# Kernel optimization log

Measured on AMD Instinct MI355X. Metric: run time of the kernel, lower is better.

Reference implementation:

```python
import jax, jax.numpy as jnp
import numpy as np

B, T, D = 4, 4096, 1024
P = 64  # d_model / n_head

def setup_inputs() -> dict:
    key = jax.random.key(0)
    k1, k2, k3 = jax.random.split(key, 3)
    x = jax.random.normal(k1, (B, T, D), dtype=jnp.float32)
    Wqkv = jax.random.normal(k2, (D, 3 * P), dtype=jnp.float32) * (1.0 / np.sqrt(D))
    bqkv = jax.random.normal(k3, (3 * P,), dtype=jnp.float32) * 0.01
    return {"x": x, "Wqkv": Wqkv, "bqkv": bqkv}

def reference(x, Wqkv, bqkv):
    Bv, Tv, Cv = x.shape
    qkv = (x @ Wqkv + bqkv).reshape(Bv, Tv, 3, P)  # [B,T,3,p]
    q, k, v = qkv[:, :, 0, :], qkv[:, :, 1, :], qkv[:, :, 2, :]
    # raw scores (source applies NO 1/sqrt(p) scaling)
    S = jnp.einsum('btp,bsp->bts', q, k)  # [B,T,T]
    causal = jnp.tril(jnp.ones((Tv, Tv), dtype=bool))
    S = jnp.where(causal[None, :, :], S, jnp.float32(-jnp.inf))
    Pm = jax.nn.softmax(S, axis=-1)
    O = jnp.einsum('bts,bsp->btp', Pm, v)  # [B,T,p]
    return O
```

## Files before the change

kernel.cpp:

```cpp
#include <hip/hip_runtime.h>
#include <hip/hip_fp16.h>

#define B_ 4
#define T_ 4096
#define D_ 1024

typedef _Float16 h8 __attribute__((ext_vector_type(8)));
typedef _Float16 h4 __attribute__((ext_vector_type(4)));
typedef float f32x4 __attribute__((ext_vector_type(4)));

#define LOG2E 1.44269504088896340736f
#define MASKV -3.0e38f
#define MINIT -1.0e30f
#define EXP2(x) __builtin_amdgcn_exp2f(x)

__global__ __launch_bounds__(256) void wt_kernel(const float* __restrict__ W,
                                                 _Float16* __restrict__ Wt) {
    __shared__ _Float16 Tr[192][20];
    const int tid = threadIdx.x, k0 = blockIdx.x * 16;
#pragma unroll
    for (int i = 0; i < 3; i++) {
        int fi = tid + 256 * i;
        int r = fi / 48, c4 = fi % 48;
        float4 v = *(const float4*)(W + (size_t)(k0 + r) * 192 + c4 * 4);
        Tr[c4 * 4 + 0][r] = (_Float16)v.x;
        Tr[c4 * 4 + 1][r] = (_Float16)v.y;
        Tr[c4 * 4 + 2][r] = (_Float16)v.z;
        Tr[c4 * 4 + 3][r] = (_Float16)v.w;
    }
    __syncthreads();
#pragma unroll
    for (int i = 0; i < 3; i++) {
        int oi = tid + 256 * i;
        int n = oi >> 2, kq = oi & 3;
        *(h4*)(Wt + (size_t)n * D_ + k0 + kq * 4) = *(const h4*)&Tr[n][kq * 4];
    }
}

__global__ __launch_bounds__(256) void proj_kernel(
    const float* __restrict__ x, const _Float16* __restrict__ Wt,
    const float* __restrict__ bias,
    _Float16* __restrict__ qh, _Float16* __restrict__ kh, _Float16* __restrict__ vh)
{
    __shared__ _Float16 As[2][32][40];
    __shared__ _Float16 Bs[2][192][40];
    __shared__ _Float16 Ost[32][200];
    const int tid = threadIdx.x;
    const int w = tid >> 6, lane = tid & 63, quad = lane >> 4, l16 = lane & 15;
    const int row0 = blockIdx.x * 32;
    const int mstrip = w & 1;
    const int ngrp = (w >> 1) * 6;

    float bvals[6];
#pragma unroll
    for (int nt = 0; nt < 6; nt++) bvals[nt] = bias[(ngrp + nt) * 16 + l16];

    f32x4 acc[6];
#pragma unroll
    for (int i = 0; i < 6; i++) acc[i] = (f32x4){0.f, 0.f, 0.f, 0.f};

    const int arow = tid >> 3, ac0 = (tid & 7) * 4;

    float4 xa;
    h8 wreg[3];
    {
        xa = *(const float4*)(x + (size_t)(row0 + arow) * D_ + ac0);
#pragma unroll
        for (int p = 0; p < 3; p++) {
            int f = tid + 256 * p; int n = f >> 2, c0 = (f & 3) * 8;
            wreg[p] = *(const h8*)(Wt + (size_t)n * D_ + c0);
        }
    }

    for (int kc = 0; kc < 32; kc++) {
        const int buf = kc & 1;
        h4 av;
        av[0]=(_Float16)xa.x; av[1]=(_Float16)xa.y; av[2]=(_Float16)xa.z; av[3]=(_Float16)xa.w;
        *(h4*)&As[buf][arow][ac0] = av;
#pragma unroll
        for (int p = 0; p < 3; p++) {
            int f = tid + 256 * p; int n = f >> 2, c0 = (f & 3) * 8;
            *(h8*)&Bs[buf][n][c0] = wreg[p];
        }
        if (kc + 1 < 32) {
            int k0 = (kc + 1) * 32;
            xa = *(const float4*)(x + (size_t)(row0 + arow) * D_ + k0 + ac0);
#pragma unroll
            for (int p = 0; p < 3; p++) {
                int f = tid + 256 * p; int n = f >> 2, c0 = (f & 3) * 8;
                wreg[p] = *(const h8*)(Wt + (size_t)n * D_ + k0 + c0);
            }
        }
        __syncthreads();
        h8 a0 = *(const h8*)&As[buf][16 * mstrip + l16][quad * 8];
#pragma unroll
        for (int nt = 0; nt < 6; nt++) {
            h8 b0 = *(const h8*)&Bs[buf][(ngrp + nt) * 16 + l16][quad * 8];
            acc[nt] = __builtin_amdgcn_mfma_f32_16x16x32_f16(a0, b0, acc[nt], 0, 0, 0);
        }
    }

#pragma unroll
    for (int nt = 0; nt < 6; nt++) {
        int n = (ngrp + nt) * 16 + l16;
        float scale = (n < 64) ? LOG2E : 1.0f;
#pragma unroll
        for (int reg = 0; reg < 4; reg++)
            Ost[16 * mstrip + quad * 4 + reg][n] =
                (_Float16)((acc[nt][reg] + bvals[nt]) * scale);
    }
    __syncthreads();
    {
        const int mrow = tid >> 3, c0 = (tid & 7) * 8;
        _Float16* dsts[3] = {qh, kh, vh};
#pragma unroll
        for (int g = 0; g < 3; g++)
            *(h8*)(dsts[g] + (size_t)(row0 + mrow) * 64 + c0) =
                *(const h8*)&Ost[mrow][g * 64 + c0];
    }
}

__global__ __launch_bounds__(256, 4) void attn_kernel(
    const _Float16* __restrict__ qh, const _Float16* __restrict__ kh,
    const _Float16* __restrict__ vh, float* __restrict__ out,
    _Float16* __restrict__ Opart, float2* __restrict__ ml,
    int lgC, int NC1, int direct, int q8, int total)
{
    __shared__ _Float16 Ks[2][64][72];
    __shared__ _Float16 Vt[2][64][72];
    const int tid = threadIdx.x;
    const int w = tid >> 6, lane = tid & 63, quad = lane >> 4, l16 = lane & 15;
    const int C = 1 << lgC;

    const int bid = blockIdx.x;
    const int cid = (bid & 7) * q8 + (bid >> 3);
    if (cid >= total) return;

    const int b = cid / NC1;
    int rem = cid - b * NC1;
    int qt2 = 0, k0 = 0, cnt = 1;
    for (int i = 0; i < 32; i++) {
        int nc = (2 * i + 2 + C - 1) >> lgC;
        if (rem < nc) { qt2 = i; k0 = rem << lgC; cnt = min(C, 2 * i + 2 - k0); break; }
        rem -= nc;
    }
    const size_t base = (size_t)b * T_ * 64;
    const int qbase = qt2 * 128 + w * 32;

    h8 qf[2][2];
#pragma unroll
    for (int u = 0; u < 2; u++) {
        const _Float16* qp = qh + base + (size_t)(qbase + u * 16 + l16) * 64 + quad * 8;
        qf[u][0] = *(const h8*)qp;
        qf[u][1] = *(const h8*)(qp + 32);
    }

    f32x4 o[8];
#pragma unroll
    for (int i = 0; i < 8; i++) o[i] = (f32x4){0.f, 0.f, 0.f, 0.f};
    float m[2] = {MINIT, MINIT}, l[2] = {0.f, 0.f};

    const int krow = tid >> 3, kc0 = (tid & 7) * 8;
    const int vp0 = (tid & 15) * 4, vc0 = (tid >> 4) * 4;
    h8 kreg[2];
    h4 vreg[4];
    {
        const _Float16* kp = kh + base + (size_t)(k0 * 64) * 64;
        kreg[0] = *(const h8*)(kp + (size_t)krow * 64 + kc0);
        kreg[1] = *(const h8*)(kp + (size_t)(krow + 32) * 64 + kc0);
        const _Float16* vp = vh + base + (size_t)(k0 * 64 + vc0) * 64 + vp0;
#pragma unroll
        for (int i = 0; i < 4; i++) vreg[i] = *(const h4*)(vp + (size_t)i * 64);
    }

    const int kend = k0 + cnt;
    for (int kt = k0; kt < kend; kt++) {
        const int buf = kt & 1;
        *(h8*)&Ks[buf][krow][kc0] = kreg[0];
        *(h8*)&Ks[buf][krow + 32][kc0] = kreg[1];
#pragma unroll
        for (int j = 0; j < 4; j++) {
            h4 t;
            t[0] = vreg[0][j]; t[1] = vreg[1][j]; t[2] = vreg[2][j]; t[3] = vreg[3][j];
            *(h4*)&Vt[buf][vp0 + j][vc0] = t;
        }
        if (kt + 1 < kend) {
            const _Float16* kp = kh + base + (size_t)((kt + 1) * 64) * 64;
            kreg[0] = *(const h8*)(kp + (size_t)krow * 64 + kc0);
            kreg[1] = *(const h8*)(kp + (size_t)(krow + 32) * 64 + kc0);
            const _Float16* vp = vh + base + (size_t)((kt + 1) * 64 + vc0) * 64 + vp0;
#pragma unroll
            for (int i = 0; i < 4; i++) vreg[i] = *(const h4*)(vp + (size_t)i * 64);
        }
        __syncthreads();

        const bool skip = (kt * 64) > (qbase + 31);
        if (!skip) {
            f32x4 s[2][4];
#pragma unroll
            for (int nt = 0; nt < 4; nt++) {
                h8 kf0 = *(const h8*)&Ks[buf][nt * 16 + l16][quad * 8];
                h8 kf1 = *(const h8*)&Ks[buf][nt * 16 + l16][32 + quad * 8];
#pragma unroll
                for (int u = 0; u < 2; u++) {
                    f32x4 c = (f32x4){0.f, 0.f, 0.f, 0.f};
                    c = __builtin_amdgcn_mfma_f32_16x16x32_f16(kf0, qf[u][0], c, 0, 0, 0);
                    c = __builtin_amdgcn_mfma_f32_16x16x32_f16(kf1, qf[u][1], c, 0, 0, 0);
                    s[u][nt] = c;
                }
            }

            h4 pf[2][4];
#pragma unroll
            for (int u = 0; u < 2; u++) {
                const int qrow = qbase + u * 16 + l16;
                if (kt * 64 + 63 > qbase + u * 16) {
#pragma unroll
                    for (int nt = 0; nt < 4; nt++)
#pragma unroll
                        for (int reg = 0; reg < 4; reg++) {
                            int sg = kt * 64 + nt * 16 + quad * 4 + reg;
                            if (sg > qrow) s[u][nt][reg] = MASKV;
                        }
                }
                float mx = s[u][0][0];
#pragma unroll
                for (int nt = 0; nt < 4; nt++)
#pragma unroll
                    for (int reg = 0; reg < 4; reg++) mx = fmaxf(mx, s[u][nt][reg]);
                mx = fmaxf(mx, __shfl_xor(mx, 16));
                mx = fmaxf(mx, __shfl_xor(mx, 32));
                float mnew = fmaxf(m[u], mx);
                float alpha = EXP2(m[u] - mnew);
                m[u] = mnew;
                float rs = 0.f;
#pragma unroll
                for (int nt = 0; nt < 4; nt++) {
#pragma unroll
                    for (int reg = 0; reg < 4; reg++) {
                        float p = EXP2(s[u][nt][reg] - mnew);
                        s[u][nt][reg] = p;
                        rs += p;
                    }
                    h4 ph;
                    ph[0]=(_Float16)s[u][nt][0]; ph[1]=(_Float16)s[u][nt][1];
                    ph[2]=(_Float16)s[u][nt][2]; ph[3]=(_Float16)s[u][nt][3];
                    pf[u][nt] = ph;
                }
                rs += __shfl_xor(rs, 16);
                rs += __shfl_xor(rs, 32);
                l[u] = l[u] * alpha + rs;
#pragma unroll
                for (int pt = 0; pt < 4; pt++)
#pragma unroll
                    for (int reg = 0; reg < 4; reg++) o[u * 4 + pt][reg] *= alpha;
            }

#pragma unroll
            for (int pt = 0; pt < 4; pt++)
#pragma unroll
                for (int nt = 0; nt < 4; nt++) {
                    h4 vf = *(const h4*)&Vt[buf][pt * 16 + l16][nt * 16 + quad * 4];
                    o[pt]     = __builtin_amdgcn_mfma_f32_16x16x16f16(vf, pf[0][nt], o[pt], 0, 0, 0);
                    o[4 + pt] = __builtin_amdgcn_mfma_f32_16x16x16f16(vf, pf[1][nt], o[4 + pt], 0, 0, 0);
                }
        }
    }

    if (direct) {
#pragma unroll
        for (int u = 0; u < 2; u++) {
            float linv = 1.0f / l[u];
            int trow = qt2 * 128 + w * 32 + u * 16 + l16;
#pragma unroll
            for (int pt = 0; pt < 4; pt++)
#pragma unroll
                for (int reg = 0; reg < 4; reg++)
                    out[base + (size_t)trow * 64 + pt * 16 + quad * 4 + reg] =
                        o[u * 4 + pt][reg] * linv;
        }
    } else {
        __syncthreads();
        _Float16* St = &Ks[0][0][0];
#pragma unroll
        for (int u = 0; u < 2; u++) {
            int r = w * 32 + u * 16 + l16;
#pragma unroll
            for (int pt = 0; pt < 4; pt++) {
                h4 ph;
#pragma unroll
                for (int reg = 0; reg < 4; reg++) ph[reg] = (_Float16)o[u * 4 + pt][reg];
                *(h4*)&St[r * 72 + pt * 16 + quad * 4] = ph;
            }
            if (quad == 0) ml[(size_t)cid * 128 + r] = make_float2(m[u], l[u]);
        }
        __syncthreads();
        _Float16* op = Opart + (size_t)cid * 8192;
        const int r = tid >> 1, c0 = (tid & 1) * 32;
#pragma unroll
        for (int j = 0; j < 4; j++)
            *(h8*)(op + r * 64 + c0 + 8 * j) = *(const h8*)&St[r * 72 + c0 + 8 * j];
    }
}

__global__ __launch_bounds__(256) void combine_kernel(
    const _Float16* __restrict__ Opart, const float2* __restrict__ ml,
    float* __restrict__ out, int lgC, int NC1)
{
    const int C = 1 << lgC;
    const int task = blockIdx.x;
    const int b = task >> 8, tile = (task >> 3) & 31, rg = task & 7;
    int pref = 0;
    for (int i = 0; i < tile; i++) pref += (2 * i + 2 + C - 1) >> lgC;
    const int cbase = b * NC1 + pref;
    const int nch = (2 * tile + 2 + C - 1) >> lgC;

    const int r = rg * 16 + (threadIdx.x >> 4);
    const int c0 = (threadIdx.x & 15) * 4;

    float M = MINIT;
    for (int i = 0; i < nch; i++) M = fmaxf(M, ml[(size_t)(cbase + i) * 128 + r].x);
    float L = 0.f, acc[4] = {0.f, 0.f, 0.f, 0.f};
    for (int i = 0; i < nch; i++) {
        float2 v = ml[(size_t)(cbase + i) * 128 + r];
        float sc = EXP2(v.x - M);
        L += sc * v.y;
        h4 x4 = *(const h4*)(Opart + (size_t)(cbase + i) * 8192 + (size_t)r * 64 + c0);
#pragma unroll
        for (int t = 0; t < 4; t++) acc[t] += sc * (float)x4[t];
    }
    float inv = 1.0f / L;
    float4 res = { acc[0]*inv, acc[1]*inv, acc[2]*inv, acc[3]*inv };
    *(float4*)(out + ((size_t)b * T_ + tile * 128 + r) * 64 + c0) = res;
}

extern "C" void kernel_launch(void* const* d_in, const int* in_sizes, int n_in,
                              void* d_out, int out_size, void* d_ws, size_t ws_size,
                              hipStream_t stream) {
    const float* x    = (const float*)d_in[0];
    const float* W    = (const float*)d_in[1];
    const float* bias = (const float*)d_in[2];
    float* out = (float*)d_out;
    char* ws = (char*)d_ws;
    _Float16* qh = (_Float16*)(ws);
    _Float16* kh = (_Float16*)(ws + (size_t)2 * 1024 * 1024);
    _Float16* vh = (_Float16*)(ws + (size_t)4 * 1024 * 1024);
    _Float16* Wt = (_Float16*)(ws + (size_t)6 * 1024 * 1024);
    const size_t pbase = (size_t)8 * 1024 * 1024;

    int lgC = -1, nc1 = 32;
    for (int lg = 3; lg <= 6; lg++) {
        int C = 1 << lg, n1 = 0;
        for (int i = 0; i < 32; i++) n1 += (2 * i + 2 + C - 1) >> lg;
        size_t need = pbase + (size_t)4 * n1 * (8192 * 2 + 128 * 8);
        if (need <= ws_size) { lgC = lg; nc1 = n1; break; }
    }
    int direct = (lgC < 0) ? 1 : 0;
    if (direct) { lgC = 6; nc1 = 32; }
    _Float16* Opart = (_Float16*)(ws + pbase);
    float2*   mlp   = (float2*)(ws + pbase + (size_t)4 * nc1 * 8192 * 2);

    const int total = 4 * nc1;
    const int q8 = (total + 7) / 8;

    wt_kernel<<<64, 256, 0, stream>>>(W, Wt);
    proj_kernel<<<512, 256, 0, stream>>>(x, Wt, bias, qh, kh, vh);
    attn_kernel<<<8 * q8, 256, 0, stream>>>(qh, kh, vh, out, Opart, mlp,
                                            lgC, nc1, direct, q8, total);
    if (!direct)
        combine_kernel<<<1024, 256, 0, stream>>>(Opart, mlp, out, lgC, nc1);
}
```

Before: 166.6 us.

## Shrink attention query tile to 64 rows and load K fragments directly into registers

The attention kernel now gives each block 64 query rows (16 per wave) instead of 128, removes the shared-memory K buffer, and has each lane load its K MFMA fragments straight from global memory with a one-tile register prefetch. Split-KV chunking, the partial-output layout and the combine kernel are reindexed for 64-row tiles, and the chunk-size search now starts at 4 tiles. This is meant to cut LDS traffic and the K staging stores, balance the causal work more finely and allow more blocks. In exchange, each K tile is read from global or L2 by every wave instead of once per block, and each block covers fewer query rows, so K/V reuse drops.

```diff
diff --git a/kernel.cpp b/kernel.cpp
--- a/kernel.cpp
+++ b/kernel.cpp
@@ -126,7 +126,6 @@
     _Float16* __restrict__ Opart, float2* __restrict__ ml,
     int lgC, int NC1, int direct, int q8, int total)
 {
-    __shared__ _Float16 Ks[2][64][72];
     __shared__ _Float16 Vt[2][64][72];
     const int tid = threadIdx.x;
     const int w = tid >> 6, lane = tid & 63, quad = lane >> 4, l16 = lane & 15;
@@ -138,46 +137,49 @@
 
     const int b = cid / NC1;
     int rem = cid - b * NC1;
-    int qt2 = 0, k0 = 0, cnt = 1;
-    for (int i = 0; i < 32; i++) {
-        int nc = (2 * i + 2 + C - 1) >> lgC;
-        if (rem < nc) { qt2 = i; k0 = rem << lgC; cnt = min(C, 2 * i + 2 - k0); break; }
+    int qt = 0, k0 = 0, cnt = 1;
+    for (int q = 0; q < 64; q++) {
+        int nc = (q + C) >> lgC;
+        if (rem < nc) { qt = q; k0 = rem << lgC; cnt = min(C, q + 1 - k0); break; }
         rem -= nc;
     }
     const size_t base = (size_t)b * T_ * 64;
-    const int qbase = qt2 * 128 + w * 32;
-
-    h8 qf[2][2];
-#pragma unroll
-    for (int u = 0; u < 2; u++) {
-        const _Float16* qp = qh + base + (size_t)(qbase + u * 16 + l16) * 64 + quad * 8;
-        qf[u][0] = *(const h8*)qp;
-        qf[u][1] = *(const h8*)(qp + 32);
-    }
-
-    f32x4 o[8];
-#pragma unroll
-    for (int i = 0; i < 8; i++) o[i] = (f32x4){0.f, 0.f, 0.f, 0.f};
-    float m[2] = {MINIT, MINIT}, l[2] = {0.f, 0.f};
-
-    const int krow = tid >> 3, kc0 = (tid & 7) * 8;
+    const int qbase = qt * 64 + w * 16;
+
+    h8 qf[2];
+    {
+        const _Float16* qp = qh + base + (size_t)(qbase + l16) * 64 + quad * 8;
+        qf[0] = *(const h8*)qp;
+        qf[1] = *(const h8*)(qp + 32);
+    }
+
+    f32x4 o[4];
+#pragma unroll
+    for (int i = 0; i < 4; i++) o[i] = (f32x4){0.f, 0.f, 0.f, 0.f};
+    float m = MINIT, l = 0.f;
+
     const int vp0 = (tid & 15) * 4, vc0 = (tid >> 4) * 4;
-    h8 kreg[2];
     h4 vreg[4];
     {
-        const _Float16* kp = kh + base + (size_t)(k0 * 64) * 64;
-        kreg[0] = *(const h8*)(kp + (size_t)krow * 64 + kc0);
-        kreg[1] = *(const h8*)(kp + (size_t)(krow + 32) * 64 + kc0);
         const _Float16* vp = vh + base + (size_t)(k0 * 64 + vc0) * 64 + vp0;
 #pragma unroll
         for (int i = 0; i < 4; i++) vreg[i] = *(const h4*)(vp + (size_t)i * 64);
+    }
+
+    const _Float16* kbase = kh + base + (size_t)l16 * 64 + quad * 8;
+    h8 kf[4][2];
+    {
+        const _Float16* kp = kbase + (size_t)k0 * 64 * 64;
+#pragma unroll
+        for (int nt = 0; nt < 4; nt++) {
+            kf[nt][0] = *(const h8*)(kp + (size_t)nt * 16 * 64);
+            kf[nt][1] = *(const h8*)(kp + (size_t)nt * 16 * 64 + 32);
+        }
     }
 
     const int kend = k0 + cnt;
     for (int kt = k0; kt < kend; kt++) {
         const int buf = kt & 1;
-        *(h8*)&Ks[buf][krow][kc0] = kreg[0];
-        *(h8*)&Ks[buf][krow + 32][kc0] = kreg[1];
 #pragma unroll
         for (int j = 0; j < 4; j++) {
             h4 t;
@@ -185,121 +187,108 @@
             *(h4*)&Vt[buf][vp0 + j][vc0] = t;
         }
         if (kt + 1 < kend) {
-            const _Float16* kp = kh + base + (size_t)((kt + 1) * 64) * 64;
-            kreg[0] = *(const h8*)(kp + (size_t)krow * 64 + kc0);
-            kreg[1] = *(const h8*)(kp + (size_t)(krow + 32) * 64 + kc0);
             const _Float16* vp = vh + base + (size_t)((kt + 1) * 64 + vc0) * 64 + vp0;
 #pragma unroll
             for (int i = 0; i < 4; i++) vreg[i] = *(const h4*)(vp + (size_t)i * 64);
         }
         __syncthreads();
 
-        const bool skip = (kt * 64) > (qbase + 31);
-        if (!skip) {
-            f32x4 s[2][4];
+        f32x4 s[4];
+#pragma unroll
+        for (int nt = 0; nt < 4; nt++) {
+            f32x4 c = (f32x4){0.f, 0.f, 0.f, 0.f};
+            c = __builtin_amdgcn_mfma_f32_16x16x32_f16(kf[nt][0], qf[0], c, 0, 0, 0);
+            c = __builtin_amdgcn_mfma_f32_16x16x32_f16(kf[nt][1], qf[1], c, 0, 0, 0);
+            s[nt] = c;
+        }
+        if (kt + 1 < kend) {
+            const _Float16* kp = kbase + (size_t)(kt + 1) * 64 * 64;
 #pragma unroll
             for (int nt = 0; nt < 4; nt++) {
-                h8 kf0 = *(const h8*)&Ks[buf][nt * 16 + l16][quad * 8];
-                h8 kf1 = *(const h8*)&Ks[buf][nt * 16 + l16][32 + quad * 8];
-#pragma unroll
-                for (int u = 0; u < 2; u++) {
-                    f32x4 c = (f32x4){0.f, 0.f, 0.f, 0.f};
-                    c = __builtin_amdgcn_mfma_f32_16x16x32_f16(kf0, qf[u][0], c, 0, 0, 0);
-                    c = __builtin_amdgcn_mfma_f32_16x16x32_f16(kf1, qf[u][1], c, 0, 0, 0);
-                    s[u][nt] = c;
+                kf[nt][0] = *(const h8*)(kp + (size_t)nt * 16 * 64);
+                kf[nt][1] = *(const h8*)(kp + (size_t)nt * 16 * 64 + 32);
+            }
+        }
+
+        if (kt == qt) {
+            const int qrow = w * 16 + l16;
+#pragma unroll
+            for (int nt = 0; nt < 4; nt++)
+#pragma unroll
+                for (int reg = 0; reg < 4; reg++) {
+                    int sg = nt * 16 + quad * 4 + reg;
+                    if (sg > qrow) s[nt][reg] = MASKV;
                 }
-            }
-
-            h4 pf[2][4];
-#pragma unroll
-            for (int u = 0; u < 2; u++) {
-                const int qrow = qbase + u * 16 + l16;
-                if (kt * 64 + 63 > qbase + u * 16) {
-#pragma unroll
-                    for (int nt = 0; nt < 4; nt++)
-#pragma unroll
-                        for (int reg = 0; reg < 4; reg++) {
-                            int sg = kt * 64 + nt * 16 + quad * 4 + reg;
-                            if (sg > qrow) s[u][nt][reg] = MASKV;
-                        }
-                }
-                float mx = s[u][0][0];
-#pragma unroll
-                for (int nt = 0; nt < 4; nt++)
-#pragma unroll
-                    for (int reg = 0; reg < 4; reg++) mx = fmaxf(mx, s[u][nt][reg]);
-                mx = fmaxf(mx, __shfl_xor(mx, 16));
-                mx = fmaxf(mx, __shfl_xor(mx, 32));
-                float mnew = fmaxf(m[u], mx);
-                float alpha = EXP2(m[u] - mnew);
-                m[u] = mnew;
-                float rs = 0.f;
-#pragma unroll
-                for (int nt = 0; nt < 4; nt++) {
-#pragma unroll
-                    for (int reg = 0; reg < 4; reg++) {
-                        float p = EXP2(s[u][nt][reg] - mnew);
-                        s[u][nt][reg] = p;
-                        rs += p;
-                    }
-                    h4 ph;
-                    ph[0]=(_Float16)s[u][nt][0]; ph[1]=(_Float16)s[u][nt][1];
-                    ph[2]=(_Float16)s[u][nt][2]; ph[3]=(_Float16)s[u][nt][3];
-                    pf[u][nt] = ph;
-                }
-                rs += __shfl_xor(rs, 16);
-                rs += __shfl_xor(rs, 32);
-                l[u] = l[u] * alpha + rs;
-#pragma unroll
-                for (int pt = 0; pt < 4; pt++)
-#pragma unroll
-                    for (int reg = 0; reg < 4; reg++) o[u * 4 + pt][reg] *= alpha;
-            }
-
-#pragma unroll
-            for (int pt = 0; pt < 4; pt++)
-#pragma unroll
-                for (int nt = 0; nt < 4; nt++) {
-                    h4 vf = *(const h4*)&Vt[buf][pt * 16 + l16][nt * 16 + quad * 4];
-                    o[pt]     = __builtin_amdgcn_mfma_f32_16x16x16f16(vf, pf[0][nt], o[pt], 0, 0, 0);
-                    o[4 + pt] = __builtin_amdgcn_mfma_f32_16x16x16f16(vf, pf[1][nt], o[4 + pt], 0, 0, 0);
-                }
-        }
+        }
+
+        float mx = s[0][0];
+#pragma unroll
+        for (int nt = 0; nt < 4; nt++)
+#pragma unroll
+            for (int reg = 0; reg < 4; reg++) mx = fmaxf(mx, s[nt][reg]);
+        mx = fmaxf(mx, __shfl_xor(mx, 16));
+        mx = fmaxf(mx, __shfl_xor(mx, 32));
+        float mnew = fmaxf(m, mx);
+        float alpha = EXP2(m - mnew);
+        m = mnew;
+        float rs = 0.f;
+        h4 pf[4];
+#pragma unroll
+        for (int nt = 0; nt < 4; nt++) {
+            h4 ph;
+#pragma unroll
+            for (int reg = 0; reg < 4; reg++) {
+                float p = EXP2(s[nt][reg] - mnew);
+                rs += p;
+                ph[reg] = (_Float16)p;
+            }
+            pf[nt] = ph;
+        }
+        rs += __shfl_xor(rs, 16);
+        rs += __shfl_xor(rs, 32);
+        l = l * alpha + rs;
+#pragma unroll
+        for (int pt = 0; pt < 4; pt++)
+#pragma unroll
+            for (int reg = 0; reg < 4; reg++) o[pt][reg] *= alpha;
+
+#pragma unroll
+        for (int pt = 0; pt < 4; pt++)
+#pragma unroll
+            for (int nt = 0; nt < 4; nt++) {
+                h4 vf = *(const h4*)&Vt[buf][pt * 16 + l16][nt * 16 + quad * 4];
+                o[pt] = __builtin_amdgcn_mfma_f32_16x16x16f16(vf, pf[nt], o[pt], 0, 0, 0);
+            }
     }
 
     if (direct) {
-#pragma unroll
-        for (int u = 0; u < 2; u++) {
-            float linv = 1.0f / l[u];
-            int trow = qt2 * 128 + w * 32 + u * 16 + l16;
-#pragma unroll
-            for (int pt = 0; pt < 4; pt++)
-#pragma unroll
-                for (int reg = 0; reg < 4; reg++)
-                    out[base + (size_t)trow * 64 + pt * 16 + quad * 4 + reg] =
-                        o[u * 4 + pt][reg] * linv;
-        }
+        float linv = 1.0f / l;
+        int trow = qt * 64 + w * 16 + l16;
+#pragma unroll
+        for (int pt = 0; pt < 4; pt++)
+#pragma unroll
+            for (int reg = 0; reg < 4; reg++)
+                out[base + (size_t)trow * 64 + pt * 16 + quad * 4 + reg] =
+                    o[pt][reg] * linv;
     } else {
         __syncthreads();
-        _Float16* St = &Ks[0][0][0];
-#pragma unroll
-        for (int u = 0; u < 2; u++) {
-            int r = w * 32 + u * 16 + l16;
+        _Float16* St = &Vt[0][0][0];
+        {
+            int r = w * 16 + l16;
 #pragma unroll
             for (int pt = 0; pt < 4; pt++) {
                 h4 ph;
 #pragma unroll
-                for (int reg = 0; reg < 4; reg++) ph[reg] = (_Float16)o[u * 4 + pt][reg];
+                for (int reg = 0; reg < 4; reg++) ph[reg] = (_Float16)o[pt][reg];
                 *(h4*)&St[r * 72 + pt * 16 + quad * 4] = ph;
             }
-            if (quad == 0) ml[(size_t)cid * 128 + r] = make_float2(m[u], l[u]);
+            if (quad == 0) ml[(size_t)cid * 64 + r] = make_float2(m, l);
         }
         __syncthreads();
-        _Float16* op = Opart + (size_t)cid * 8192;
-        const int r = tid >> 1, c0 = (tid & 1) * 32;
-#pragma unroll
-        for (int j = 0; j < 4; j++)
-            *(h8*)(op + r * 64 + c0 + 8 * j) = *(const h8*)&St[r * 72 + c0 + 8 * j];
+        _Float16* op = Opart + (size_t)cid * 4096;
+        const int r = tid >> 2, c0 = (tid & 3) * 16;
+        *(h8*)(op + r * 64 + c0)     = *(const h8*)&St[r * 72 + c0];
+        *(h8*)(op + r * 64 + c0 + 8) = *(const h8*)&St[r * 72 + c0 + 8];
     }
 }
 
@@ -309,29 +298,29 @@
 {
     const int C = 1 << lgC;
     const int task = blockIdx.x;
-    const int b = task >> 8, tile = (task >> 3) & 31, rg = task & 7;
+    const int b = task >> 8, qt = (task >> 2) & 63, rg = task & 3;
     int pref = 0;
-    for (int i = 0; i < tile; i++) pref += (2 * i + 2 + C - 1) >> lgC;
+    for (int q = 0; q < qt; q++) pref += (q + C) >> lgC;
     const int cbase = b * NC1 + pref;
-    const int nch = (2 * tile + 2 + C - 1) >> lgC;
+    const int nch = (qt + C) >> lgC;
 
     const int r = rg * 16 + (threadIdx.x >> 4);
     const int c0 = (threadIdx.x & 15) * 4;
 
     float M = MINIT;
-    for (int i = 0; i < nch; i++) M = fmaxf(M, ml[(size_t)(cbase + i) * 128 + r].x);
+    for (int i = 0; i < nch; i++) M = fmaxf(M, ml[(size_t)(cbase + i) * 64 + r].x);
     float L = 0.f, acc[4] = {0.f, 0.f, 0.f, 0.f};
     for (int i = 0; i < nch; i++) {
-        float2 v = ml[(size_t)(cbase + i) * 128 + r];
+        float2 v = ml[(size_t)(cbase + i) * 64 + r];
         float sc = EXP2(v.x - M);
         L += sc * v.y;
-        h4 x4 = *(const h4*)(Opart + (size_t)(cbase + i) * 8192 + (size_t)r * 64 + c0);
+        h4 x4 = *(const h4*)(Opart + (size_t)(cbase + i) * 4096 + (size_t)r * 64 + c0);
 #pragma unroll
         for (int t = 0; t < 4; t++) acc[t] += sc * (float)x4[t];
     }
     float inv = 1.0f / L;
     float4 res = { acc[0]*inv, acc[1]*inv, acc[2]*inv, acc[3]*inv };
-    *(float4*)(out + ((size_t)b * T_ + tile * 128 + r) * 64 + c0) = res;
+    *(float4*)(out + ((size_t)b * T_ + qt * 64 + r) * 64 + c0) = res;
 }
 
 extern "C" void kernel_launch(void* const* d_in, const int* in_sizes, int n_in,
@@ -348,17 +337,17 @@
     _Float16* Wt = (_Float16*)(ws + (size_t)6 * 1024 * 1024);
     const size_t pbase = (size_t)8 * 1024 * 1024;
 
-    int lgC = -1, nc1 = 32;
-    for (int lg = 3; lg <= 6; lg++) {
+    int lgC = -1, nc1 = 64;
+    for (int lg = 2; lg <= 6; lg++) {
         int C = 1 << lg, n1 = 0;
-        for (int i = 0; i < 32; i++) n1 += (2 * i + 2 + C - 1) >> lg;
-        size_t need = pbase + (size_t)4 * n1 * (8192 * 2 + 128 * 8);
+        for (int q = 0; q < 64; q++) n1 += (q + C) >> lg;
+        size_t need = pbase + (size_t)4 * n1 * (4096 * 2 + 64 * 8);
         if (need <= ws_size) { lgC = lg; nc1 = n1; break; }
     }
     int direct = (lgC < 0) ? 1 : 0;
-    if (direct) { lgC = 6; nc1 = 32; }
+    if (direct) { lgC = 6; nc1 = 64; }
     _Float16* Opart = (_Float16*)(ws + pbase);
-    float2*   mlp   = (float2*)(ws + pbase + (size_t)4 * nc1 * 8192 * 2);
+    float2*   mlp   = (float2*)(ws + pbase + (size_t)4 * nc1 * 4096 * 2);
 
     const int total = 4 * nc1;
     const int q8 = (total + 7) / 8;
```

After: 174.6 us. 1.05x slower.

## Load K fragments directly into registers, drop K LDS staging, alias proj LDS

Applied to the files above, without the earlier changes.

In the attention kernel, K tiles are now read from global memory straight into MFMA fragment registers (kf[4][2]) and prefetched for the next tile, so the shared-memory K buffer and its LDS writes and reads go away. Attention LDS drops to the V-transpose buffer only, which may allow higher occupancy. The split-reduction chunk search now starts at chunk size 4, producing more and smaller partial work items. The projection kernel reuses its A/B staging LDS for the output staging buffer, adding one barrier. The costs are duplicated K global loads across waves, which now rely on cache, and more reduction partials.

```diff
diff --git a/kernel.cpp b/kernel.cpp
--- a/kernel.cpp
+++ b/kernel.cpp
@@ -42,9 +42,10 @@
     const float* __restrict__ bias,
     _Float16* __restrict__ qh, _Float16* __restrict__ kh, _Float16* __restrict__ vh)
 {
-    __shared__ _Float16 As[2][32][40];
-    __shared__ _Float16 Bs[2][192][40];
-    __shared__ _Float16 Ost[32][200];
+    __shared__ __align__(16) char psm[35840];
+    _Float16* Asp = (_Float16*)psm;
+    _Float16* Bsp = (_Float16*)(psm + 5120);
+    _Float16* Ostp = (_Float16*)psm;
     const int tid = threadIdx.x;
     const int w = tid >> 6, lane = tid & 63, quad = lane >> 4, l16 = lane & 15;
     const int row0 = blockIdx.x * 32;
@@ -76,11 +77,11 @@
         const int buf = kc & 1;
         h4 av;
         av[0]=(_Float16)xa.x; av[1]=(_Float16)xa.y; av[2]=(_Float16)xa.z; av[3]=(_Float16)xa.w;
-        *(h4*)&As[buf][arow][ac0] = av;
+        *(h4*)(Asp + buf * 1280 + arow * 40 + ac0) = av;
 #pragma unroll
         for (int p = 0; p < 3; p++) {
             int f = tid + 256 * p; int n = f >> 2, c0 = (f & 3) * 8;
-            *(h8*)&Bs[buf][n][c0] = wreg[p];
+            *(h8*)(Bsp + buf * 7680 + n * 40 + c0) = wreg[p];
         }
         if (kc + 1 < 32) {
             int k0 = (kc + 1) * 32;
@@ -92,21 +93,22 @@
             }
         }
         __syncthreads();
-        h8 a0 = *(const h8*)&As[buf][16 * mstrip + l16][quad * 8];
+        h8 a0 = *(const h8*)(Asp + buf * 1280 + (16 * mstrip + l16) * 40 + quad * 8);
 #pragma unroll
         for (int nt = 0; nt < 6; nt++) {
-            h8 b0 = *(const h8*)&Bs[buf][(ngrp + nt) * 16 + l16][quad * 8];
+            h8 b0 = *(const h8*)(Bsp + buf * 7680 + ((ngrp + nt) * 16 + l16) * 40 + quad * 8);
             acc[nt] = __builtin_amdgcn_mfma_f32_16x16x32_f16(a0, b0, acc[nt], 0, 0, 0);
         }
     }
 
+    __syncthreads();
 #pragma unroll
     for (int nt = 0; nt < 6; nt++) {
         int n = (ngrp + nt) * 16 + l16;
         float scale = (n < 64) ? LOG2E : 1.0f;
 #pragma unroll
         for (int reg = 0; reg < 4; reg++)
-            Ost[16 * mstrip + quad * 4 + reg][n] =
+            Ostp[(16 * mstrip + quad * 4 + reg) * 200 + n] =
                 (_Float16)((acc[nt][reg] + bvals[nt]) * scale);
     }
     __syncthreads();
@@ -116,7 +118,7 @@
 #pragma unroll
         for (int g = 0; g < 3; g++)
             *(h8*)(dsts[g] + (size_t)(row0 + mrow) * 64 + c0) =
-                *(const h8*)&Ost[mrow][g * 64 + c0];
+                *(const h8*)(Ostp + mrow * 200 + g * 64 + c0);
     }
 }
 
@@ -126,7 +128,6 @@
     _Float16* __restrict__ Opart, float2* __restrict__ ml,
     int lgC, int NC1, int direct, int q8, int total)
 {
-    __shared__ _Float16 Ks[2][64][72];
     __shared__ _Float16 Vt[2][64][72];
     const int tid = threadIdx.x;
     const int w = tid >> 6, lane = tid & 63, quad = lane >> 4, l16 = lane & 15;
@@ -160,24 +161,28 @@
     for (int i = 0; i < 8; i++) o[i] = (f32x4){0.f, 0.f, 0.f, 0.f};
     float m[2] = {MINIT, MINIT}, l[2] = {0.f, 0.f};
 
-    const int krow = tid >> 3, kc0 = (tid & 7) * 8;
     const int vp0 = (tid & 15) * 4, vc0 = (tid >> 4) * 4;
-    h8 kreg[2];
     h4 vreg[4];
     {
-        const _Float16* kp = kh + base + (size_t)(k0 * 64) * 64;
-        kreg[0] = *(const h8*)(kp + (size_t)krow * 64 + kc0);
-        kreg[1] = *(const h8*)(kp + (size_t)(krow + 32) * 64 + kc0);
         const _Float16* vp = vh + base + (size_t)(k0 * 64 + vc0) * 64 + vp0;
 #pragma unroll
         for (int i = 0; i < 4; i++) vreg[i] = *(const h4*)(vp + (size_t)i * 64);
+    }
+
+    const _Float16* kbase = kh + base + (size_t)l16 * 64 + quad * 8;
+    h8 kf[4][2];
+    {
+        const _Float16* kp = kbase + (size_t)k0 * 4096;
+#pragma unroll
+        for (int nt = 0; nt < 4; nt++) {
+            kf[nt][0] = *(const h8*)(kp + (size_t)nt * 1024);
+            kf[nt][1] = *(const h8*)(kp + (size_t)nt * 1024 + 32);
+        }
     }
 
     const int kend = k0 + cnt;
     for (int kt = k0; kt < kend; kt++) {
         const int buf = kt & 1;
-        *(h8*)&Ks[buf][krow][kc0] = kreg[0];
-        *(h8*)&Ks[buf][krow + 32][kc0] = kreg[1];
 #pragma unroll
         for (int j = 0; j < 4; j++) {
             h4 t;
@@ -185,9 +190,6 @@
             *(h4*)&Vt[buf][vp0 + j][vc0] = t;
         }
         if (kt + 1 < kend) {
-            const _Float16* kp = kh + base + (size_t)((kt + 1) * 64) * 64;
-            kreg[0] = *(const h8*)(kp + (size_t)krow * 64 + kc0);
-            kreg[1] = *(const h8*)(kp + (size_t)(krow + 32) * 64 + kc0);
             const _Float16* vp = vh + base + (size_t)((kt + 1) * 64 + vc0) * 64 + vp0;
 #pragma unroll
             for (int i = 0; i < 4; i++) vreg[i] = *(const h4*)(vp + (size_t)i * 64);
@@ -196,23 +198,17 @@
 
         const bool skip = (kt * 64) > (qbase + 31);
         if (!skip) {
-            f32x4 s[2][4];
-#pragma unroll
-            for (int nt = 0; nt < 4; nt++) {
-                h8 kf0 = *(const h8*)&Ks[buf][nt * 16 + l16][quad * 8];
-                h8 kf1 = *(const h8*)&Ks[buf][nt * 16 + l16][32 + quad * 8];
-#pragma unroll
-                for (int u = 0; u < 2; u++) {
+            h4 pf[2][4];
+#pragma unroll
+            for (int u = 0; u < 2; u++) {
+                f32x4 s[4];
+#pragma unroll
+                for (int nt = 0; nt < 4; nt++) {
                     f32x4 c = (f32x4){0.f, 0.f, 0.f, 0.f};
-                    c = __builtin_amdgcn_mfma_f32_16x16x32_f16(kf0, qf[u][0], c, 0, 0, 0);
-                    c = __builtin_amdgcn_mfma_f32_16x16x32_f16(kf1, qf[u][1], c, 0, 0, 0);
-                    s[u][nt] = c;
-                }
-            }
-
-            h4 pf[2][4];
-#pragma unroll
-            for (int u = 0; u < 2; u++) {
+                    c = __builtin_amdgcn_mfma_f32_16x16x32_f16(kf[nt][0], qf[u][0], c, 0, 0, 0);
+                    c = __builtin_amdgcn_mfma_f32_16x16x32_f16(kf[nt][1], qf[u][1], c, 0, 0, 0);
+                    s[nt] = c;
+                }
                 const int qrow = qbase + u * 16 + l16;
                 if (kt * 64 + 63 > qbase + u * 16) {
 #pragma unroll
@@ -220,14 +216,14 @@
 #pragma unroll
                         for (int reg = 0; reg < 4; reg++) {
                             int sg = kt * 64 + nt * 16 + quad * 4 + reg;
-                            if (sg > qrow) s[u][nt][reg] = MASKV;
+                            if (sg > qrow) s[nt][reg] = MASKV;
                         }
                 }
-                float mx = s[u][0][0];
+                float mx = s[0][0];
 #pragma unroll
                 for (int nt = 0; nt < 4; nt++)
 #pragma unroll
-                    for (int reg = 0; reg < 4; reg++) mx = fmaxf(mx, s[u][nt][reg]);
+                    for (int reg = 0; reg < 4; reg++) mx = fmaxf(mx, s[nt][reg]);
                 mx = fmaxf(mx, __shfl_xor(mx, 16));
                 mx = fmaxf(mx, __shfl_xor(mx, 32));
                 float mnew = fmaxf(m[u], mx);
@@ -236,15 +232,13 @@
                 float rs = 0.f;
 #pragma unroll
                 for (int nt = 0; nt < 4; nt++) {
+                    h4 ph;
 #pragma unroll
                     for (int reg = 0; reg < 4; reg++) {
-                        float p = EXP2(s[u][nt][reg] - mnew);
-                        s[u][nt][reg] = p;
+                        float p = EXP2(s[nt][reg] - mnew);
                         rs += p;
+                        ph[reg] = (_Float16)p;
                     }
-                    h4 ph;
-                    ph[0]=(_Float16)s[u][nt][0]; ph[1]=(_Float16)s[u][nt][1];
-                    ph[2]=(_Float16)s[u][nt][2]; ph[3]=(_Float16)s[u][nt][3];
                     pf[u][nt] = ph;
                 }
                 rs += __shfl_xor(rs, 16);
@@ -254,6 +248,15 @@
                 for (int pt = 0; pt < 4; pt++)
 #pragma unroll
                     for (int reg = 0; reg < 4; reg++) o[u * 4 + pt][reg] *= alpha;
+            }
+
+            if (kt + 1 < kend) {
+                const _Float16* kp = kbase + (size_t)(kt + 1) * 4096;
+#pragma unroll
+                for (int nt = 0; nt < 4; nt++) {
+                    kf[nt][0] = *(const h8*)(kp + (size_t)nt * 1024);
+                    kf[nt][1] = *(const h8*)(kp + (size_t)nt * 1024 + 32);
+                }
             }
 
 #pragma unroll
@@ -264,6 +267,13 @@
                     o[pt]     = __builtin_amdgcn_mfma_f32_16x16x16f16(vf, pf[0][nt], o[pt], 0, 0, 0);
                     o[4 + pt] = __builtin_amdgcn_mfma_f32_16x16x16f16(vf, pf[1][nt], o[4 + pt], 0, 0, 0);
                 }
+        } else if (kt + 1 < kend) {
+            const _Float16* kp = kbase + (size_t)(kt + 1) * 4096;
+#pragma unroll
+            for (int nt = 0; nt < 4; nt++) {
+                kf[nt][0] = *(const h8*)(kp + (size_t)nt * 1024);
+                kf[nt][1] = *(const h8*)(kp + (size_t)nt * 1024 + 32);
+            }
         }
     }
 
@@ -281,7 +291,7 @@
         }
     } else {
         __syncthreads();
-        _Float16* St = &Ks[0][0][0];
+        _Float16* St = &Vt[0][0][0];
 #pragma unroll
         for (int u = 0; u < 2; u++) {
             int r = w * 32 + u * 16 + l16;
@@ -349,7 +359,7 @@
     const size_t pbase = (size_t)8 * 1024 * 1024;
 
     int lgC = -1, nc1 = 32;
-    for (int lg = 3; lg <= 6; lg++) {
+    for (int lg = 2; lg <= 6; lg++) {
         int C = 1 << lg, n1 = 0;
         for (int i = 0; i < 32; i++) n1 += (2 * i + 2 + C - 1) >> lg;
         size_t need = pbase + (size_t)4 * n1 * (8192 * 2 + 128 * 8);
```

Result: slower. 218.9 us (+31.4%).
